# Kernel tuning notes

Measured on AMD Instinct MI355X. Metric: run time of the kernel, lower is better.

Reference implementation:

```python
import jax, jax.numpy as jnp
import numpy as np
from jax import lax

B, T, V, E, H = 32, 512, 32000, 300, 256
TRANSITION = 0.1
TEMP = 0.01
BUDGET_PCT = 30.0
NEG = -1e9


def setup_inputs() -> dict:
    key = jax.random.key(0)
    ks = jax.random.split(key, 10)
    sc = lambda k, shape, s=0.05: (jax.random.normal(k, shape, jnp.float32) * s)
    x = jax.random.randint(ks[0], (B, T), 0, V)
    mask = jnp.ones((B, T), bool)
    embed = sc(ks[1], (V, E), 0.1)
    w_ih_f = sc(ks[2], (E, 4 * H))
    w_hh_f = sc(ks[3], (H, 4 * H))
    b_f = jnp.zeros((4 * H,), jnp.float32)
    w_ih_b = sc(ks[4], (E, 4 * H))
    w_hh_b = sc(ks[5], (H, 4 * H))
    b_b = jnp.zeros((4 * H,), jnp.float32)
    w_out = sc(ks[6], (2 * H, 1), 0.1)
    b_out = jnp.zeros((1,), jnp.float32)
    return {"x": x, "current_epoch": 0, "mask": mask, "embed": embed,
            "w_ih_f": w_ih_f, "w_hh_f": w_hh_f, "b_f": b_f,
            "w_ih_b": w_ih_b, "w_hh_b": w_hh_b, "b_b": b_b,
            "w_out": w_out, "b_out": b_out}


def _lstm_dir(emb, mask, Wi, Wh, b):
    # masked LSTM equivalent to pack_padded_sequence; gate order i,f,g,o (torch)
    bs, tl, _ = emb.shape
    h0 = jnp.zeros((bs, Wh.shape[0]), emb.dtype)
    xg = emb @ Wi + b  # [B,T,4H]

    def step(carry, inp):
        h, c = carry
        xg_t, m_t = inp
        g = xg_t + h @ Wh
        i, f, gg, o = jnp.split(g, 4, axis=-1)
        i = jax.nn.sigmoid(i); f = jax.nn.sigmoid(f)
        gg = jnp.tanh(gg); o = jax.nn.sigmoid(o)
        c_new = f * c + i * gg
        h_new = o * jnp.tanh(c_new)
        m = m_t[:, None]
        h_new = jnp.where(m, h_new, h)
        c_new = jnp.where(m, c_new, c)
        return (h_new, c_new), jnp.where(m, h_new, 0.0)

    _, hs = lax.scan(step, (h0, h0), (xg.transpose(1, 0, 2), mask.T))
    return hs.transpose(1, 0, 2)


def _forward(x, mask, embed, w_ih_f, w_hh_f, b_f, w_ih_b, w_hh_b, b_b, w_out, b_out):
    emb = embed[x]  # [B,T,E] (dropout disabled / eval)
    h_f = _lstm_dir(emb, mask, w_ih_f, w_hh_f, b_f)
    h_b = jnp.flip(_lstm_dir(jnp.flip(emb, 1), jnp.flip(mask, 1), w_ih_b, w_hh_b, b_b), 1)
    h = jnp.concatenate([h_f, h_b], axis=-1)  # [B,T,2H]
    scores = (h @ w_out + b_out)[..., 0]  # [B,T]

    lengths = mask.sum(1)
    pos = jnp.arange(T)
    # unary for state 0 (selected); padded positions forced off
    u0 = jnp.where(pos[None, :] < lengths[:, None], scores / TEMP, NEG)
    # transition[t,0,0] = transition/temp for t <= length, else 0;  t in 0..T
    tvals = jnp.where(jnp.arange(T + 1)[None, :] <= lengths[:, None], TRANSITION / TEMP, 0.0)
    budget = jnp.round(BUDGET_PCT / 100.0 * lengths)
    Cmax = int(round(BUDGET_PCT / 100.0 * T)) + 1  # static count dim

    def logZ(u0_):
        alpha = jnp.full((u0_.shape[0], Cmax, 2), NEG, u0_.dtype)
        alpha = alpha.at[:, 1, 0].set(u0_[:, 0] + tvals[:, 0])  # start in state0 (count 1)
        alpha = alpha.at[:, 0, 1].set(0.0)                       # start in state1 (count 0)

        def step(a, inp):
            u0_t, t_t = inp
            a_shift = jnp.concatenate([jnp.full((a.shape[0], 1, 2), NEG, a.dtype), a[:, :-1, :]], axis=1)
            m0 = jnp.logaddexp(a_shift[..., 0] + t_t[:, None], a_shift[..., 1])
            m1 = jnp.logaddexp(a[..., 0], a[..., 1])
            return jnp.stack([u0_t[:, None] + m0, m1], axis=-1), None

        alpha, _ = lax.scan(step, alpha, (u0_[:, 1:].T, tvals[:, 1:T].T))
        final = jnp.stack([alpha[..., 0] + tvals[:, T][:, None], alpha[..., 1]], axis=-1)
        allowed = (jnp.arange(Cmax)[None, :] <= budget[:, None])[..., None]
        lz = jax.nn.logsumexp(jnp.where(allowed, final, NEG).reshape(final.shape[0], -1), axis=-1)
        return lz.sum()

    # marginal p(z_i=1) = d logZ / d u0_i  (budget-constrained chain marginals)
    z = jax.grad(logZ)(u0)
    return jnp.where(mask, z, 0.0)


def reference(x, current_epoch, mask, embed, w_ih_f, w_hh_f, b_f, w_ih_b, w_hh_b, b_b, w_out, b_out):
    return _forward(x, mask, embed, w_ih_f, w_hh_f, b_f, w_ih_b, w_hh_b, b_b, w_out, b_out)
```

## Files before the change

### kernel.cpp

```cpp
#include <hip/hip_runtime.h>
#include <math.h>

#define BB 32
#define TT_LEN 512
#define EE 300
#define KPAD 320
#define HH 256
#define G4 1024
#define CMAX 155
#define TRANS_T 10.0f
#define NEGF -1.0e9f
#define INV_TEMP 100.0f
#define AST_STRIDE 159

#define NCH_L2 8
#define NREG 24

typedef _Float16 half2v __attribute__((ext_vector_type(2)));
typedef _Float16 half8 __attribute__((ext_vector_type(8)));
typedef float f32x4 __attribute__((ext_vector_type(4)));

__device__ __forceinline__ float la(float x, float y) {
  float m = fmaxf(x, y);
  float d = fminf(x, y) - m;
  return m + __logf(1.0f + __expf(d));
}

__device__ __forceinline__ float sigm(float x) {
  return 1.0f / (1.0f + __expf(-x));
}

__device__ __forceinline__ float dot2acc(unsigned int wd, unsigned int hd, float acc) {
#if __has_builtin(__builtin_amdgcn_fdot2)
  return __builtin_amdgcn_fdot2(__builtin_bit_cast(half2v, wd),
                                __builtin_bit_cast(half2v, hd), acc, false);
#else
  half2v a = __builtin_bit_cast(half2v, wd);
  half2v b = __builtin_bit_cast(half2v, hd);
  return acc + (float)a.x * (float)b.x + (float)a.y * (float)b.y;
#endif
}

__device__ __forceinline__ unsigned int packh(float a, float b) {
  half2v hp;
  hp.x = (_Float16)a;
  hp.y = (_Float16)b;
  return __builtin_bit_cast(unsigned int, hp);
}

__global__ void prep_weights(const float* wi_f, const float* wi_b,
                             const float* wh_f, const float* wh_b,
                             const float* b_f, const float* b_b,
                             unsigned int* wi_frag, float* b_p,
                             unsigned int* wlds_h, unsigned int* wstr_h) {
  int idx = blockIdx.x * blockDim.x + threadIdx.x;
  int stride = gridDim.x * blockDim.x;
  for (int i = idx; i < 2 * 64 * 10 * 64 * 4; i += stride) {
    int u4 = i >> 2, d = i & 3;
    int lane = u4 & 63;
    int kk = (u4 >> 6) % 10;
    int nb = (u4 / 640) & 63;
    int dir = u4 / (640 * 64);
    int l15 = lane & 15, quad = lane >> 4;
    int n = nb * 16 + l15;
    int g = n & 3, u = n >> 2;
    int k0 = kk * 32 + quad * 8 + 2 * d;
    const float* src = dir ? wi_b : wi_f;
    float v0 = (k0 < EE) ? src[(size_t)k0 * G4 + g * HH + u] : 0.0f;
    float v1 = (k0 + 1 < EE) ? src[(size_t)(k0 + 1) * G4 + g * HH + u] : 0.0f;
    wi_frag[i] = packh(v0, v1);
  }
  for (int i = idx; i < 2 * NCH_L2 * 4096; i += stride) {
    int dir = i / (NCH_L2 * 4096);
    int r = i % (NCH_L2 * 4096);
    int c = r / 4096;
    int r2 = r % 4096;
    int j = r2 >> 2, d = r2 & 3;
    int g = j & 3, u = j >> 2;
    int k0 = 8 * c + 2 * d;
    const float* src = dir ? wh_b : wh_f;
    wlds_h[i] = packh(src[k0 * G4 + g * HH + u], src[(k0 + 1) * G4 + g * HH + u]);
  }
  for (int i = idx; i < 2 * NREG * 4096; i += stride) {
    int dir = i / (NREG * 4096);
    int r = i % (NREG * 4096);
    int gch = r / 4096;
    int r2 = r % 4096;
    int j = r2 >> 2, d = r2 & 3;
    int g = j & 3, u = j >> 2;
    int k0 = 64 + 8 * gch + 2 * d;
    const float* src = dir ? wh_b : wh_f;
    wstr_h[i] = packh(src[k0 * G4 + g * HH + u], src[(k0 + 1) * G4 + g * HH + u]);
  }
  for (int i = idx; i < 2 * G4; i += stride) {
    int dir = i / G4;
    int j = i % G4;
    int g = j & 3, u = j >> 2;
    const float* src = dir ? b_b : b_f;
    b_p[i] = src[g * HH + u];
  }
}

__global__ void gather_emb(const int* x, const float* embed, uint4* emb_frag) {
  int mblk = blockIdx.x;
  int t = threadIdx.x;
  __shared__ int xs[16];
  if (t < 16) xs[t] = x[mblk * 16 + t];
  __syncthreads();
  for (int slot = t; slot < 640; slot += 256) {
    int kk = slot >> 6;
    int lane = slot & 63;
    int l15 = lane & 15, quad = lane >> 4;
    int row = xs[l15];
    int kbase = kk * 32 + quad * 8;
    const float* src = embed + (size_t)row * EE;
    float v[8];
#pragma unroll
    for (int e = 0; e < 8; ++e) v[e] = (kbase + e < EE) ? src[kbase + e] : 0.0f;
    uint4 o;
    o.x = packh(v[0], v[1]);
    o.y = packh(v[2], v[3]);
    o.z = packh(v[4], v[5]);
    o.w = packh(v[6], v[7]);
    emb_frag[(size_t)(mblk * 10 + kk) * 64 + lane] = o;
  }
}

__global__ __launch_bounds__(256) void xg_mfma(
    const uint4* __restrict__ emb_frag, const uint4* __restrict__ wi_frag,
    const float* __restrict__ b_p, float* __restrict__ xg) {
  int dir = blockIdx.z;
  int w = threadIdx.x >> 6;
  int lane = threadIdx.x & 63;
  int l15 = lane & 15, quad = lane >> 4;
  int mblk = blockIdx.y * 4 + w;

  const uint4* abase = emb_frag + (size_t)mblk * 10 * 64 + lane;
  f32x4 acc[4];
#pragma unroll
  for (int nt = 0; nt < 4; ++nt) acc[nt] = (f32x4){0.f, 0.f, 0.f, 0.f};

#pragma unroll
  for (int kk = 0; kk < 10; ++kk) {
    half8 a = __builtin_bit_cast(half8, abase[kk * 64]);
#pragma unroll
    for (int nt = 0; nt < 4; ++nt) {
      int nb = blockIdx.x * 4 + nt;
      half8 b = __builtin_bit_cast(
          half8, wi_frag[((size_t)(dir * 64 + nb) * 10 + kk) * 64 + lane]);
      acc[nt] = __builtin_amdgcn_mfma_f32_16x16x32_f16(a, b, acc[nt], 0, 0, 0);
    }
  }
#pragma unroll
  for (int nt = 0; nt < 4; ++nt) {
    int n = (blockIdx.x * 4 + nt) * 16 + l15;
    float bias = b_p[dir * G4 + n];
#pragma unroll
    for (int r = 0; r < 4; ++r) {
      int m = mblk * 16 + quad * 4 + r;
      xg[((size_t)dir * (BB * TT_LEN) + m) * G4 + n] = acc[nt][r] + bias;
    }
  }
}

__global__ __launch_bounds__(512, 2) void lstm_ck(
    const float* __restrict__ xg, const unsigned int* __restrict__ wlds_h,
    const uint4* __restrict__ wstr, const float* __restrict__ w_out,
    float* __restrict__ scores_part, float* __restrict__ hst,
    float* __restrict__ cst, int s0i, int s1i) {
  int bid = blockIdx.x;
  int dir = bid >> 5, b = bid & 31;
  int t = threadIdx.x;
  int lane = t & 63, wid = t >> 6;

  __shared__ uint4 wlds[NCH_L2 * 1024];
  __shared__ uint4 hpk4[32];
  __shared__ float gates[1024];
  __shared__ float wpart[2][4];

  const uint4* wsrcl = (const uint4*)wlds_h + (size_t)dir * (NCH_L2 * 1024);
  for (int i = t; i < NCH_L2 * 1024; i += 512) wlds[i] = wsrcl[i];
  const uint4* wsb = wstr + (size_t)dir * (NREG * 1024);
  uint4 wr0[NREG], wr1[NREG];
#pragma unroll
  for (int g = 0; g < NREG; ++g) {
    wr0[g] = wsb[g * 1024 + t];
    wr1[g] = wsb[g * 1024 + t + 512];
  }
  if (t < 32)
    hpk4[t] = (s0i == 0) ? uint4{0, 0, 0, 0} : ((const uint4*)hst)[bid * 32 + t];
  float cstate = 0.0f;
  if (s0i > 0 && t < HH) cstate = cst[bid * HH + t];
  __syncthreads();

  const float* xgbase =
      xg + (size_t)(dir * (BB * TT_LEN) + b * TT_LEN) * G4 + t;
  float wo = (t < HH) ? w_out[dir * HH + t] : 0.0f;

  int t0 = dir ? (TT_LEN - 1 - s0i) : s0i;
  float xgn0 = xgbase[(size_t)t0 * G4];
  float xgn1 = xgbase[(size_t)t0 * G4 + 512];

#pragma unroll 1
  for (int s = s0i; s < s1i; ++s) {
    int tt = dir ? (TT_LEN - 1 - s) : s;
    float acc0a = xgn0, acc1a = xgn1;
    float acc0b = 0.0f, acc1b = 0.0f;
    if (s + 1 < TT_LEN) {
      int t2 = dir ? (TT_LEN - 2 - s) : (s + 1);
      xgn0 = xgbase[(size_t)t2 * G4];
      xgn1 = xgbase[(size_t)t2 * G4 + 512];
    }
#pragma unroll
    for (int c = 0; c < NCH_L2; ++c) {
      uint4 h = hpk4[c];
      uint4 w0 = wlds[c * 1024 + t];
      uint4 w1 = wlds[c * 1024 + 512 + t];
      acc0a = dot2acc(w0.x, h.x, acc0a);
      acc0a = dot2acc(w0.y, h.y, acc0a);
      acc0a = dot2acc(w0.z, h.z, acc0a);
      acc0a = dot2acc(w0.w, h.w, acc0a);
      acc1a = dot2acc(w1.x, h.x, acc1a);
      acc1a = dot2acc(w1.y, h.y, acc1a);
      acc1a = dot2acc(w1.z, h.z, acc1a);
      acc1a = dot2acc(w1.w, h.w, acc1a);
    }
#pragma unroll
    for (int g = 0; g < NREG; ++g) {
      uint4 h = hpk4[NCH_L2 + g];
      if (g < 12) {
        acc0a = dot2acc(wr0[g].x, h.x, acc0a);
        acc0a = dot2acc(wr0[g].y, h.y, acc0a);
        acc0a = dot2acc(wr0[g].z, h.z, acc0a);
        acc0a = dot2acc(wr0[g].w, h.w, acc0a);
        acc1a = dot2acc(wr1[g].x, h.x, acc1a);
        acc1a = dot2acc(wr1[g].y, h.y, acc1a);
        acc1a = dot2acc(wr1[g].z, h.z, acc1a);
        acc1a = dot2acc(wr1[g].w, h.w, acc1a);
      } else {
        acc0b = dot2acc(wr0[g].x, h.x, acc0b);
        acc0b = dot2acc(wr0[g].y, h.y, acc0b);
        acc0b = dot2acc(wr0[g].z, h.z, acc0b);
        acc0b = dot2acc(wr0[g].w, h.w, acc0b);
        acc1b = dot2acc(wr1[g].x, h.x, acc1b);
        acc1b = dot2acc(wr1[g].y, h.y, acc1b);
        acc1b = dot2acc(wr1[g].z, h.z, acc1b);
        acc1b = dot2acc(wr1[g].w, h.w, acc1b);
      }
    }
    gates[t] = acc0a + acc0b;
    gates[512 + t] = acc1a + acc1b;
    __syncthreads();

    if (t < HH) {
      float4 g4 = ((const float4*)gates)[t];
      float ig = sigm(g4.x);
      float fg = sigm(g4.y);
      float gg = tanhf(g4.z);
      float og = sigm(g4.w);
      cstate = fg * cstate + ig * gg;
      float h = og * tanhf(cstate);
      float prod = h * wo;
#pragma unroll
      for (int off = 32; off > 0; off >>= 1) prod += __shfl_down(prod, off, 64);
      if (lane == 0) wpart[s & 1][wid] = prod;
      float hn = __shfl_down(h, 1, 64);
      if (!(t & 1)) ((unsigned int*)hpk4)[t >> 1] = packh(h, hn);
    }
    __syncthreads();
    if (t == 0) {
      scores_part[(size_t)(dir * BB + b) * TT_LEN + tt] =
          wpart[s & 1][0] + wpart[s & 1][1] + wpart[s & 1][2] + wpart[s & 1][3];
    }
  }
  if (t < 32) ((uint4*)hst)[bid * 32 + t] = hpk4[t];
  if (t < HH) cst[bid * HH + t] = cstate;
}

__global__ __launch_bounds__(64) void dp2(const float* __restrict__ scores_part,
                                          const float* __restrict__ b_out,
                                          float* __restrict__ ast_g,
                                          float* __restrict__ out) {
  int b = blockIdx.x;
  int l = threadIdx.x;
  const float* spf = scores_part + (size_t)b * TT_LEN;
  const float* spb = scores_part + (size_t)(BB + b) * TT_LEN;
  float bo = b_out[0];
  float* ast = ast_g + (size_t)b * TT_LEN * AST_STRIDE;

  float ur[8];
#pragma unroll
  for (int i = 0; i < 8; ++i)
    ur[i] = (spf[i * 64 + l] + spb[i * 64 + l] + bo) * INV_TEMP;

  int lm1 = (l + 63) & 63;
  int lp1 = (l + 1) & 63;

  float a0[3], a1[3];
  float u00 = __shfl(ur[0], 0, 64);
  a0[0] = (l == 1) ? (u00 + TRANS_T) : NEGF;
  a0[1] = NEGF;
  a0[2] = NEGF;
  a1[0] = (l == 0) ? 0.0f : NEGF;
  a1[1] = NEGF;
  a1[2] = NEGF;
  ast[l] = a0[0];
  ast[64 + l] = a0[1];
  if (l < 27) ast[128 + l] = a0[2];

#pragma unroll
  for (int ch = 0; ch < 8; ++ch) {
    float uc = ur[ch];
#pragma unroll 1
    for (int tt = (ch == 0 ? 1 : 0); tt < 64; ++tt) {
      int t = ch * 64 + tt;
      float u0t = __shfl(uc, tt, 64);
      float w0a = __shfl(a0[0], lm1, 64);
      float w1a = __shfl(a0[1], lm1, 64);
      float w2a = __shfl(a0[2], lm1, 64);
      float w0b = __shfl(a1[0], lm1, 64);
      float w1b = __shfl(a1[1], lm1, 64);
      float w2b = __shfl(a1[2], lm1, 64);
      float p0a = (l == 0) ? NEGF : w0a;
      float p1a = (l == 0) ? w0a : w1a;
      float p2a = (l == 0) ? w1a : w2a;
      float p0b = (l == 0) ? NEGF : w0b;
      float p1b = (l == 0) ? w0b : w1b;
      float p2b = (l == 0) ? w1b : w2b;
      float n00 = u0t + la(p0a + TRANS_T, p0b);
      float n01 = u0t + la(p1a + TRANS_T, p1b);
      float n02 = u0t + la(p2a + TRANS_T, p2b);
      float n10 = la(a0[0], a1[0]);
      float n11 = la(a0[1], a1[1]);
      float n12 = la(a0[2], a1[2]);
      a0[0] = n00;
      a0[1] = n01;
      a0[2] = (l < 27) ? n02 : NEGF;
      a1[0] = n10;
      a1[1] = n11;
      a1[2] = (l < 27) ? n12 : NEGF;
      float* astr = ast + (size_t)t * AST_STRIDE;
      astr[l] = a0[0];
      astr[64 + l] = a0[1];
      if (l < 27) astr[128 + l] = a0[2];
    }
  }

  float f00 = a0[0] + TRANS_T, f01 = a0[1] + TRANS_T, f02 = a0[2] + TRANS_T;
  float m = fmaxf(fmaxf(fmaxf(f00, f01), fmaxf(f02, a1[0])), fmaxf(a1[1], a1[2]));
#pragma unroll
  for (int off = 32; off > 0; off >>= 1) m = fmaxf(m, __shfl_xor(m, off, 64));
  float es = __expf(f00 - m) + __expf(f01 - m) + __expf(f02 - m) +
             __expf(a1[0] - m) + __expf(a1[1] - m) + __expf(a1[2] - m);
#pragma unroll
  for (int off = 32; off > 0; off >>= 1) es += __shfl_xor(es, off, 64);
  float lz = m + __logf(es);

  float b0[3], b1[3];
  b0[0] = TRANS_T;
  b0[1] = TRANS_T;
  b0[2] = (l < 27) ? TRANS_T : NEGF;
  b1[0] = 0.0f;
  b1[1] = 0.0f;
  b1[2] = (l < 27) ? 0.0f : NEGF;
  {
    float ts = __expf(a0[0] + TRANS_T - lz) + __expf(a0[1] + TRANS_T - lz) +
               ((l < 27) ? __expf(a0[2] + TRANS_T - lz) : 0.0f);
#pragma unroll
    for (int off = 32; off > 0; off >>= 1) ts += __shfl_xor(ts, off, 64);
    if (l == 0) out[b * TT_LEN + (TT_LEN - 1)] = ts;
  }

  float nr0 = ast[(size_t)510 * AST_STRIDE + l];
  float nr1 = ast[(size_t)510 * AST_STRIDE + 64 + l];
  float nr2 = (l < 27) ? ast[(size_t)510 * AST_STRIDE + 128 + l] : NEGF;

#pragma unroll
  for (int ch = 7; ch >= 0; --ch) {
    float uc = ur[ch];
#pragma unroll 1
    for (int tt = 63; tt >= (ch == 0 ? 1 : 0); --tt) {
      int t = ch * 64 + tt;
      float u0t = __shfl(uc, tt, 64);
      float c0 = nr0, c1 = nr1, c2 = nr2;
      if (t >= 2) {
        const float* astr = ast + (size_t)(t - 2) * AST_STRIDE;
        nr0 = astr[l];
        nr1 = astr[64 + l];
        nr2 = (l < 27) ? astr[128 + l] : NEGF;
      }
      float w0 = __shfl(b0[0], lp1, 64);
      float w1 = __shfl(b0[1], lp1, 64);
      float w2 = __shfl(b0[2], lp1, 64);
      float x2 = (l == 63) ? NEGF : w2;
      float x1 = (l == 63) ? w2 : w1;
      float x0 = (l == 63) ? w1 : w0;
      float nb00 = la(u0t + TRANS_T + x0, b1[0]);
      float nb01 = la(u0t + TRANS_T + x1, b1[1]);
      float nb02 = la(u0t + TRANS_T + x2, b1[2]);
      float nb10 = la(u0t + x0, b1[0]);
      float nb11 = la(u0t + x1, b1[1]);
      float nb12 = la(u0t + x2, b1[2]);
      float tm = __expf(c0 + nb00 - lz) + __expf(c1 + nb01 - lz) +
                 ((l < 27) ? __expf(c2 + nb02 - lz) : 0.0f);
#pragma unroll
      for (int off = 32; off > 0; off >>= 1) tm += __shfl_xor(tm, off, 64);
      if (l == 0) out[b * TT_LEN + (t - 1)] = tm;
      b0[0] = nb00;
      b0[1] = nb01;
      b0[2] = (l < 27) ? nb02 : NEGF;
      b1[0] = nb10;
      b1[1] = nb11;
      b1[2] = (l < 27) ? nb12 : NEGF;
    }
  }
}

extern "C" void kernel_launch(void* const* d_in, const int* in_sizes, int n_in,
                              void* d_out, int out_size, void* d_ws, size_t ws_size,
                              hipStream_t stream) {
  const int* x = (const int*)d_in[0];
  const float* embed = (const float*)d_in[3];
  const float* wi_f = (const float*)d_in[4];
  const float* wh_f = (const float*)d_in[5];
  const float* bf = (const float*)d_in[6];
  const float* wi_b = (const float*)d_in[7];
  const float* wh_b = (const float*)d_in[8];
  const float* bbias = (const float*)d_in[9];
  const float* w_out = (const float*)d_in[10];
  const float* b_out = (const float*)d_in[11];

  float* ws = (float*)d_ws;
  float* b_p = ws;
  unsigned int* wlds_h = (unsigned int*)(b_p + 2 * G4);
  unsigned int* wstr_h = wlds_h + 2 * NCH_L2 * 4096;
  unsigned int* wi_frag = wstr_h + 2 * NREG * 4096;
  uint4* emb_frag = (uint4*)(wi_frag + 2 * 64 * 10 * 64 * 4);
  float* xg = (float*)(emb_frag + (size_t)1024 * 10 * 64);
  float* scores_part = xg + (size_t)2 * BB * TT_LEN * G4;
  float* hst = scores_part + 2 * BB * TT_LEN;
  float* cst = hst + 64 * 32 * 4;
  float* ast_g = cst + 64 * HH;
  float* outp = (float*)d_out;

  prep_weights<<<256, 256, 0, stream>>>(wi_f, wi_b, wh_f, wh_b, bf, bbias,
                                        wi_frag, b_p, wlds_h, wstr_h);
  gather_emb<<<(BB * TT_LEN) / 16, 256, 0, stream>>>(x, embed, emb_frag);
  dim3 g1(16, 256, 2);
  xg_mfma<<<g1, 256, 0, stream>>>(emb_frag, (const uint4*)wi_frag, b_p, xg);
  for (int c = 0; c < 4; ++c) {
    lstm_ck<<<64, 512, 0, stream>>>(xg, wlds_h, (const uint4*)wstr_h, w_out,
                                    scores_part, hst, cst, c * 128,
                                    (c + 1) * 128);
  }
  dp2<<<BB, 64, 0, stream>>>(scores_part, b_out, ast_g, outp);
}
```

Measured before the change: 1.893 ms.

## Run forward and backward DP passes concurrently and merge LSTM chunk launches

The budget-constrained chain DP, which previously ran the backward pass after the forward pass in a single wavefront, now runs the alpha and beta recursions in two separate wavefronts of one block. Each wavefront stores its full table, and a new marginal kernel combines the two tables with logZ in parallel across all positions. The four chunked LSTM launches become one launch over all 512 steps, so hidden and cell state no longer round-trip through global memory between chunks. The beta table reuses the embedding fragment buffer, which adds memory traffic and one extra launch, and the inner DP loops are now unrolled by 4.

Measured after the change: 1.554 ms. 17.9% less time.

```diff
diff --git a/kernel.cpp b/kernel.cpp
--- a/kernel.cpp
+++ b/kernel.cpp
@@ -4,7 +4,6 @@
 #define BB 32
 #define TT_LEN 512
 #define EE 300
-#define KPAD 320
 #define HH 256
 #define G4 1024
 #define CMAX 155
@@ -166,8 +165,7 @@
 __global__ __launch_bounds__(512, 2) void lstm_ck(
     const float* __restrict__ xg, const unsigned int* __restrict__ wlds_h,
     const uint4* __restrict__ wstr, const float* __restrict__ w_out,
-    float* __restrict__ scores_part, float* __restrict__ hst,
-    float* __restrict__ cst, int s0i, int s1i) {
+    float* __restrict__ scores_part) {
   int bid = blockIdx.x;
   int dir = bid >> 5, b = bid & 31;
   int t = threadIdx.x;
@@ -187,22 +185,20 @@
     wr0[g] = wsb[g * 1024 + t];
     wr1[g] = wsb[g * 1024 + t + 512];
   }
-  if (t < 32)
-    hpk4[t] = (s0i == 0) ? uint4{0, 0, 0, 0} : ((const uint4*)hst)[bid * 32 + t];
-  float cstate = 0.0f;
-  if (s0i > 0 && t < HH) cstate = cst[bid * HH + t];
+  if (t < 32) hpk4[t] = uint4{0, 0, 0, 0};
   __syncthreads();
 
   const float* xgbase =
       xg + (size_t)(dir * (BB * TT_LEN) + b * TT_LEN) * G4 + t;
   float wo = (t < HH) ? w_out[dir * HH + t] : 0.0f;
-
-  int t0 = dir ? (TT_LEN - 1 - s0i) : s0i;
+  float cstate = 0.0f;
+
+  int t0 = dir ? (TT_LEN - 1) : 0;
   float xgn0 = xgbase[(size_t)t0 * G4];
   float xgn1 = xgbase[(size_t)t0 * G4 + 512];
 
 #pragma unroll 1
-  for (int s = s0i; s < s1i; ++s) {
+  for (int s = 0; s < TT_LEN; ++s) {
     int tt = dir ? (TT_LEN - 1 - s) : s;
     float acc0a = xgn0, acc1a = xgn1;
     float acc0b = 0.0f, acc1b = 0.0f;
@@ -273,147 +269,152 @@
           wpart[s & 1][0] + wpart[s & 1][1] + wpart[s & 1][2] + wpart[s & 1][3];
     }
   }
-  if (t < 32) ((uint4*)hst)[bid * 32 + t] = hpk4[t];
-  if (t < HH) cst[bid * HH + t] = cstate;
-}
-
-__global__ __launch_bounds__(64) void dp2(const float* __restrict__ scores_part,
-                                          const float* __restrict__ b_out,
-                                          float* __restrict__ ast_g,
-                                          float* __restrict__ out) {
+}
+
+__global__ __launch_bounds__(128) void dp3(const float* __restrict__ scores_part,
+                                           const float* __restrict__ b_out,
+                                           float* __restrict__ ast_g,
+                                           float* __restrict__ bst_g,
+                                           float* __restrict__ lzv) {
   int b = blockIdx.x;
-  int l = threadIdx.x;
+  int l = threadIdx.x & 63;
+  int w = threadIdx.x >> 6;
   const float* spf = scores_part + (size_t)b * TT_LEN;
   const float* spb = scores_part + (size_t)(BB + b) * TT_LEN;
   float bo = b_out[0];
-  float* ast = ast_g + (size_t)b * TT_LEN * AST_STRIDE;
 
   float ur[8];
 #pragma unroll
   for (int i = 0; i < 8; ++i)
     ur[i] = (spf[i * 64 + l] + spb[i * 64 + l] + bo) * INV_TEMP;
 
-  int lm1 = (l + 63) & 63;
-  int lp1 = (l + 1) & 63;
-
-  float a0[3], a1[3];
-  float u00 = __shfl(ur[0], 0, 64);
-  a0[0] = (l == 1) ? (u00 + TRANS_T) : NEGF;
-  a0[1] = NEGF;
-  a0[2] = NEGF;
-  a1[0] = (l == 0) ? 0.0f : NEGF;
-  a1[1] = NEGF;
-  a1[2] = NEGF;
-  ast[l] = a0[0];
-  ast[64 + l] = a0[1];
-  if (l < 27) ast[128 + l] = a0[2];
-
-#pragma unroll
-  for (int ch = 0; ch < 8; ++ch) {
-    float uc = ur[ch];
-#pragma unroll 1
-    for (int tt = (ch == 0 ? 1 : 0); tt < 64; ++tt) {
-      int t = ch * 64 + tt;
-      float u0t = __shfl(uc, tt, 64);
-      float w0a = __shfl(a0[0], lm1, 64);
-      float w1a = __shfl(a0[1], lm1, 64);
-      float w2a = __shfl(a0[2], lm1, 64);
-      float w0b = __shfl(a1[0], lm1, 64);
-      float w1b = __shfl(a1[1], lm1, 64);
-      float w2b = __shfl(a1[2], lm1, 64);
-      float p0a = (l == 0) ? NEGF : w0a;
-      float p1a = (l == 0) ? w0a : w1a;
-      float p2a = (l == 0) ? w1a : w2a;
-      float p0b = (l == 0) ? NEGF : w0b;
-      float p1b = (l == 0) ? w0b : w1b;
-      float p2b = (l == 0) ? w1b : w2b;
-      float n00 = u0t + la(p0a + TRANS_T, p0b);
-      float n01 = u0t + la(p1a + TRANS_T, p1b);
-      float n02 = u0t + la(p2a + TRANS_T, p2b);
-      float n10 = la(a0[0], a1[0]);
-      float n11 = la(a0[1], a1[1]);
-      float n12 = la(a0[2], a1[2]);
-      a0[0] = n00;
-      a0[1] = n01;
-      a0[2] = (l < 27) ? n02 : NEGF;
-      a1[0] = n10;
-      a1[1] = n11;
-      a1[2] = (l < 27) ? n12 : NEGF;
-      float* astr = ast + (size_t)t * AST_STRIDE;
-      astr[l] = a0[0];
-      astr[64 + l] = a0[1];
-      if (l < 27) astr[128 + l] = a0[2];
-    }
-  }
-
-  float f00 = a0[0] + TRANS_T, f01 = a0[1] + TRANS_T, f02 = a0[2] + TRANS_T;
-  float m = fmaxf(fmaxf(fmaxf(f00, f01), fmaxf(f02, a1[0])), fmaxf(a1[1], a1[2]));
-#pragma unroll
-  for (int off = 32; off > 0; off >>= 1) m = fmaxf(m, __shfl_xor(m, off, 64));
-  float es = __expf(f00 - m) + __expf(f01 - m) + __expf(f02 - m) +
-             __expf(a1[0] - m) + __expf(a1[1] - m) + __expf(a1[2] - m);
-#pragma unroll
-  for (int off = 32; off > 0; off >>= 1) es += __shfl_xor(es, off, 64);
-  float lz = m + __logf(es);
-
-  float b0[3], b1[3];
-  b0[0] = TRANS_T;
-  b0[1] = TRANS_T;
-  b0[2] = (l < 27) ? TRANS_T : NEGF;
-  b1[0] = 0.0f;
-  b1[1] = 0.0f;
-  b1[2] = (l < 27) ? 0.0f : NEGF;
-  {
-    float ts = __expf(a0[0] + TRANS_T - lz) + __expf(a0[1] + TRANS_T - lz) +
-               ((l < 27) ? __expf(a0[2] + TRANS_T - lz) : 0.0f);
-#pragma unroll
-    for (int off = 32; off > 0; off >>= 1) ts += __shfl_xor(ts, off, 64);
-    if (l == 0) out[b * TT_LEN + (TT_LEN - 1)] = ts;
-  }
-
-  float nr0 = ast[(size_t)510 * AST_STRIDE + l];
-  float nr1 = ast[(size_t)510 * AST_STRIDE + 64 + l];
-  float nr2 = (l < 27) ? ast[(size_t)510 * AST_STRIDE + 128 + l] : NEGF;
-
-#pragma unroll
-  for (int ch = 7; ch >= 0; --ch) {
-    float uc = ur[ch];
-#pragma unroll 1
-    for (int tt = 63; tt >= (ch == 0 ? 1 : 0); --tt) {
-      int t = ch * 64 + tt;
-      float u0t = __shfl(uc, tt, 64);
-      float c0 = nr0, c1 = nr1, c2 = nr2;
-      if (t >= 2) {
-        const float* astr = ast + (size_t)(t - 2) * AST_STRIDE;
-        nr0 = astr[l];
-        nr1 = astr[64 + l];
-        nr2 = (l < 27) ? astr[128 + l] : NEGF;
+  if (w == 0) {
+    float* ast = ast_g + (size_t)b * TT_LEN * AST_STRIDE;
+    int lm1 = (l + 63) & 63;
+    float a0[3], a1[3];
+    float u00 = __shfl(ur[0], 0, 64);
+    a0[0] = (l == 1) ? (u00 + TRANS_T) : NEGF;
+    a0[1] = NEGF;
+    a0[2] = NEGF;
+    a1[0] = (l == 0) ? 0.0f : NEGF;
+    a1[1] = NEGF;
+    a1[2] = NEGF;
+    ast[l] = a0[0];
+    ast[64 + l] = a0[1];
+    if (l < 27) ast[128 + l] = a0[2];
+
+#pragma unroll
+    for (int ch = 0; ch < 8; ++ch) {
+      float uc = ur[ch];
+#pragma unroll 4
+      for (int tt = (ch == 0 ? 1 : 0); tt < 64; ++tt) {
+        int t = ch * 64 + tt;
+        float u0t = __shfl(uc, tt, 64);
+        float w0a = __shfl(a0[0], lm1, 64);
+        float w1a = __shfl(a0[1], lm1, 64);
+        float w2a = __shfl(a0[2], lm1, 64);
+        float w0b = __shfl(a1[0], lm1, 64);
+        float w1b = __shfl(a1[1], lm1, 64);
+        float w2b = __shfl(a1[2], lm1, 64);
+        float p0a = (l == 0) ? NEGF : w0a;
+        float p1a = (l == 0) ? w0a : w1a;
+        float p2a = (l == 0) ? w1a : w2a;
+        float p0b = (l == 0) ? NEGF : w0b;
+        float p1b = (l == 0) ? w0b : w1b;
+        float p2b = (l == 0) ? w1b : w2b;
+        float n00 = u0t + la(p0a + TRANS_T, p0b);
+        float n01 = u0t + la(p1a + TRANS_T, p1b);
+        float n02 = u0t + la(p2a + TRANS_T, p2b);
+        float n10 = la(a0[0], a1[0]);
+        float n11 = la(a0[1], a1[1]);
+        float n12 = la(a0[2], a1[2]);
+        a0[0] = n00;
+        a0[1] = n01;
+        a0[2] = (l < 27) ? n02 : NEGF;
+        a1[0] = n10;
+        a1[1] = n11;
+        a1[2] = (l < 27) ? n12 : NEGF;
+        float* astr = ast + (size_t)t * AST_STRIDE;
+        astr[l] = a0[0];
+        astr[64 + l] = a0[1];
+        if (l < 27) astr[128 + l] = a0[2];
       }
-      float w0 = __shfl(b0[0], lp1, 64);
-      float w1 = __shfl(b0[1], lp1, 64);
-      float w2 = __shfl(b0[2], lp1, 64);
-      float x2 = (l == 63) ? NEGF : w2;
-      float x1 = (l == 63) ? w2 : w1;
-      float x0 = (l == 63) ? w1 : w0;
-      float nb00 = la(u0t + TRANS_T + x0, b1[0]);
-      float nb01 = la(u0t + TRANS_T + x1, b1[1]);
-      float nb02 = la(u0t + TRANS_T + x2, b1[2]);
-      float nb10 = la(u0t + x0, b1[0]);
-      float nb11 = la(u0t + x1, b1[1]);
-      float nb12 = la(u0t + x2, b1[2]);
-      float tm = __expf(c0 + nb00 - lz) + __expf(c1 + nb01 - lz) +
-                 ((l < 27) ? __expf(c2 + nb02 - lz) : 0.0f);
-#pragma unroll
-      for (int off = 32; off > 0; off >>= 1) tm += __shfl_xor(tm, off, 64);
-      if (l == 0) out[b * TT_LEN + (t - 1)] = tm;
-      b0[0] = nb00;
-      b0[1] = nb01;
-      b0[2] = (l < 27) ? nb02 : NEGF;
-      b1[0] = nb10;
-      b1[1] = nb11;
-      b1[2] = (l < 27) ? nb12 : NEGF;
-    }
-  }
+    }
+    float f00 = a0[0] + TRANS_T, f01 = a0[1] + TRANS_T, f02 = a0[2] + TRANS_T;
+    float m = fmaxf(fmaxf(fmaxf(f00, f01), fmaxf(f02, a1[0])),
+                    fmaxf(a1[1], a1[2]));
+#pragma unroll
+    for (int off = 32; off > 0; off >>= 1) m = fmaxf(m, __shfl_xor(m, off, 64));
+    float es = __expf(f00 - m) + __expf(f01 - m) + __expf(f02 - m) +
+               __expf(a1[0] - m) + __expf(a1[1] - m) + __expf(a1[2] - m);
+#pragma unroll
+    for (int off = 32; off > 0; off >>= 1) es += __shfl_xor(es, off, 64);
+    if (l == 0) lzv[b] = m + __logf(es);
+  } else {
+    float* bst = bst_g + (size_t)b * TT_LEN * AST_STRIDE;
+    int lp1 = (l + 1) & 63;
+    float b0[3], b1[3];
+    b0[0] = TRANS_T;
+    b0[1] = TRANS_T;
+    b0[2] = (l < 27) ? TRANS_T : NEGF;
+    b1[0] = 0.0f;
+    b1[1] = 0.0f;
+    b1[2] = (l < 27) ? 0.0f : NEGF;
+    {
+      float* br = bst + (size_t)(TT_LEN - 1) * AST_STRIDE;
+      br[l] = b0[0];
+      br[64 + l] = b0[1];
+      if (l < 27) br[128 + l] = b0[2];
+    }
+#pragma unroll
+    for (int ch = 7; ch >= 0; --ch) {
+      float uc = ur[ch];
+#pragma unroll 4
+      for (int tt = 63; tt >= (ch == 0 ? 1 : 0); --tt) {
+        int t = ch * 64 + tt;
+        float u0t = __shfl(uc, tt, 64);
+        float w0 = __shfl(b0[0], lp1, 64);
+        float w1 = __shfl(b0[1], lp1, 64);
+        float w2 = __shfl(b0[2], lp1, 64);
+        float x2 = (l == 63) ? NEGF : w2;
+        float x1 = (l == 63) ? w2 : w1;
+        float x0 = (l == 63) ? w1 : w0;
+        float nb00 = la(u0t + TRANS_T + x0, b1[0]);
+        float nb01 = la(u0t + TRANS_T + x1, b1[1]);
+        float nb02 = la(u0t + TRANS_T + x2, b1[2]);
+        float nb10 = la(u0t + x0, b1[0]);
+        float nb11 = la(u0t + x1, b1[1]);
+        float nb12 = la(u0t + x2, b1[2]);
+        b0[0] = nb00;
+        b0[1] = nb01;
+        b0[2] = (l < 27) ? nb02 : NEGF;
+        b1[0] = nb10;
+        b1[1] = nb11;
+        b1[2] = (l < 27) ? nb12 : NEGF;
+        float* br = bst + (size_t)(t - 1) * AST_STRIDE;
+        br[l] = b0[0];
+        br[64 + l] = b0[1];
+        if (l < 27) br[128 + l] = b0[2];
+      }
+    }
+  }
+}
+
+__global__ __launch_bounds__(256) void marg(const float* __restrict__ ast_g,
+                                            const float* __restrict__ bst_g,
+                                            const float* __restrict__ lzv,
+                                            float* __restrict__ out) {
+  int row = blockIdx.x * 4 + (threadIdx.x >> 6);
+  int l = threadIdx.x & 63;
+  int b = row >> 9;
+  const float* ar = ast_g + (size_t)row * AST_STRIDE;
+  const float* br = bst_g + (size_t)row * AST_STRIDE;
+  float lz = lzv[b];
+  float s = __expf(ar[l] + br[l] - lz) + __expf(ar[64 + l] + br[64 + l] - lz) +
+            ((l < 27) ? __expf(ar[128 + l] + br[128 + l] - lz) : 0.0f);
+#pragma unroll
+  for (int off = 32; off > 0; off >>= 1) s += __shfl_xor(s, off, 64);
+  if (l == 0) out[row] = s;
 }
 
 extern "C" void kernel_launch(void* const* d_in, const int* in_sizes, int n_in,
@@ -436,11 +437,11 @@
   unsigned int* wstr_h = wlds_h + 2 * NCH_L2 * 4096;
   unsigned int* wi_frag = wstr_h + 2 * NREG * 4096;
   uint4* emb_frag = (uint4*)(wi_frag + 2 * 64 * 10 * 64 * 4);
+  float* bst_g = (float*)emb_frag;
   float* xg = (float*)(emb_frag + (size_t)1024 * 10 * 64);
   float* scores_part = xg + (size_t)2 * BB * TT_LEN * G4;
-  float* hst = scores_part + 2 * BB * TT_LEN;
-  float* cst = hst + 64 * 32 * 4;
-  float* ast_g = cst + 64 * HH;
+  float* lzv = scores_part + 2 * BB * TT_LEN;
+  float* ast_g = lzv + 64;
   float* outp = (float*)d_out;
 
   prep_weights<<<256, 256, 0, stream>>>(wi_f, wi_b, wh_f, wh_b, bf, bbias,
@@ -448,10 +449,8 @@
   gather_emb<<<(BB * TT_LEN) / 16, 256, 0, stream>>>(x, embed, emb_frag);
   dim3 g1(16, 256, 2);
   xg_mfma<<<g1, 256, 0, stream>>>(emb_frag, (const uint4*)wi_frag, b_p, xg);
-  for (int c = 0; c < 4; ++c) {
-    lstm_ck<<<64, 512, 0, stream>>>(xg, wlds_h, (const uint4*)wstr_h, w_out,
-                                    scores_part, hst, cst, c * 128,
-                                    (c + 1) * 128);
-  }
-  dp2<<<BB, 64, 0, stream>>>(scores_part, b_out, ast_g, outp);
-}
+  lstm_ck<<<64, 512, 0, stream>>>(xg, wlds_h, (const uint4*)wstr_h, w_out,
+                                  scores_part);
+  dp3<<<BB, 128, 0, stream>>>(scores_part, b_out, ast_g, bst_g, lzv);
+  marg<<<(BB * TT_LEN) / 4, 256, 0, stream>>>(ast_g, bst_g, lzv, outp);
+}
```
